# Optimization experiments

Measured on AMD Instinct MI355X. Metric: run time of the kernel, lower is better.

## Reference

```python
import jax, jax.numpy as jnp
import numpy as np


def gcn_conv(x, edge_index, W, b):
    # PyG GCNConv with normalize=True: add self-loops, symmetric D^-1/2 A D^-1/2,
    # transform then aggregate messages source->target, then add bias.
    N = x.shape[0]
    row, col = edge_index[0], edge_index[1]  # row: source, col: target
    loop = jnp.arange(N, dtype=edge_index.dtype)
    row = jnp.concatenate([row, loop])
    col = jnp.concatenate([col, loop])
    ones = jnp.ones(row.shape[0], dtype=x.dtype)
    deg = jax.ops.segment_sum(ones, col, num_segments=N)
    dinv = jnp.where(deg > 0, jax.lax.rsqrt(deg), 0.0)
    norm = dinv[row] * dinv[col]            # [E+N]
    h = x @ W                                # [N, d_out] transform first (cheaper aggregation)
    msgs = h[row] * norm[:, None]            # gather + scale
    out = jax.ops.segment_sum(msgs, col, num_segments=N)  # scatter-add to targets
    return out + b


def setup_inputs() -> dict:
    key = jax.random.key(0)
    k = jax.random.split(key, 6)
    N, D, H, C, E = 100000, 256, 32, 2, 3200000
    x = jax.random.normal(k[0], (N, D), dtype=jnp.float32)
    edge_index = jax.random.randint(k[1], (2, E), 0, N, dtype=jnp.int64)
    # glorot-style init for GCN weights
    W1 = jax.random.normal(k[2], (D, H), dtype=jnp.float32) * np.sqrt(2.0 / (D + H))
    b1 = jnp.zeros((H,), dtype=jnp.float32)
    W2 = jax.random.normal(k[3], (H, C), dtype=jnp.float32) * np.sqrt(2.0 / (H + C))
    b2 = jnp.zeros((C,), dtype=jnp.float32)
    return {"x": x, "edge_index": edge_index, "W1": W1, "b1": b1, "W2": W2, "b2": b2}


def reference(x, edge_index, W1, b1, W2, b2):
    # CRD: GCNConv -> relu -> dropout(p=0.5, eval mode -> identity)
    h = jax.nn.relu(gcn_conv(x, edge_index, W1, b1))
    # CLS: GCNConv -> log_softmax over classes
    logits = gcn_conv(h, edge_index, W2, b2)
    return jax.nn.log_softmax(logits, axis=1)
```

## Files before the change

kernel.cpp:

```cpp
#include <hip/hip_runtime.h>
#include <hip/hip_fp16.h>
#include <math.h>

#define DIV_UP(a,b) (((a)+(b)-1)/(b))

typedef _Float16 f16x8 __attribute__((ext_vector_type(8)));
typedef float    f32x4 __attribute__((ext_vector_type(4)));

#define SHIFT 9
#define TPB   (1 << SHIFT)
#define LMASK (TPB - 1)
#define CHUNK 4096

__global__ __launch_bounds__(256) void k_init(int* __restrict__ gcur, int cap,
                                              int* __restrict__ offsets, int N, int E) {
    const int t = threadIdx.x;
    gcur[t] = t * cap;
    if (t == 0) offsets[N] = E;
}

__global__ __launch_bounds__(256) void k_fat(const float* __restrict__ x,
                                             const float* __restrict__ W,
                                             __half* __restrict__ h1,
                                             const int* __restrict__ row,
                                             const int* __restrict__ col,
                                             int* __restrict__ gcur,
                                             unsigned* __restrict__ binned,
                                             int E, int N, int nchunk) {
    __shared__ __align__(16) char smem[24608];
    const int t = threadIdx.x;
    const int bid = blockIdx.x;
    const bool isBin = (bid < 2 * nchunk) && (bid & 1);

    if (!isBin) {
        const int gb = (bid < 2 * nchunk) ? (bid >> 1) : (bid - nchunk);
        _Float16* WlT = (_Float16*)smem;

#pragma unroll
        for (int i = 0; i < 8; ++i) {
            int idx = t + 256 * i;
            float4 v = ((const float4*)W)[idx];
            int k  = idx >> 3;
            int n4 = (idx & 7) * 4;
            int kc = k >> 5, q = (k >> 3) & 3, j = k & 7;
            int ct = n4 >> 4, m0 = n4 & 15;
            _Float16* dst = WlT + ((size_t)((kc * 2 + ct) * 64 + q * 16 + m0) * 8 + j);
            dst[0 * 8] = (_Float16)v.x;
            dst[1 * 8] = (_Float16)v.y;
            dst[2 * 8] = (_Float16)v.z;
            dst[3 * 8] = (_Float16)v.w;
        }
        __syncthreads();

        const int lane = t & 63;
        const int wv   = t >> 6;
        const int m    = lane & 15;
        const int q    = lane >> 4;

        const int rowA   = gb * 64 + wv * 16 + m;
        const int rclamp = min(rowA, N - 1);
        const float* xr  = x + (long long)rclamp * 256 + q * 8;

        f32x4 c0 = {0.f, 0.f, 0.f, 0.f}, c1 = {0.f, 0.f, 0.f, 0.f};
#pragma unroll
        for (int kc = 0; kc < 8; ++kc) {
            float4 v0 = *(const float4*)(xr + kc * 32);
            float4 v1 = *(const float4*)(xr + kc * 32 + 4);
            f16x8 b0 = *(const f16x8*)&WlT[(size_t)((kc * 2 + 0) * 64 + lane) * 8];
            f16x8 b1 = *(const f16x8*)&WlT[(size_t)((kc * 2 + 1) * 64 + lane) * 8];
            f16x8 a;
            a[0] = (_Float16)v0.x; a[1] = (_Float16)v0.y;
            a[2] = (_Float16)v0.z; a[3] = (_Float16)v0.w;
            a[4] = (_Float16)v1.x; a[5] = (_Float16)v1.y;
            a[6] = (_Float16)v1.z; a[7] = (_Float16)v1.w;
            c0 = __builtin_amdgcn_mfma_f32_16x16x32_f16(a, b0, c0, 0, 0, 0);
            c1 = __builtin_amdgcn_mfma_f32_16x16x32_f16(a, b1, c1, 0, 0, 0);
        }

        const int orow = gb * 64 + wv * 16 + q * 4;
#pragma unroll
        for (int r = 0; r < 4; ++r) {
            int gr = orow + r;
            if (gr < N) {
                h1[gr * 32 + m]      = __float2half(c0[r]);
                h1[gr * 32 + 16 + m] = __float2half(c1[r]);
            }
        }
    } else {
        int* hist  = (int*)smem;
        int* loff  = hist + 256;
        int* gbase = loff + 256;
        int* lcur  = gbase + 256;
        unsigned* staged     = (unsigned*)(smem + 4096);
        unsigned char* binOf = (unsigned char*)(smem + 4096 + 16384);
        int* wtot            = (int*)(smem + 4096 + 16384 + 4096);

        const int base = (bid >> 1) * CHUNK;
        const int n = min(CHUNK, E - base);

        hist[t] = 0;
        __syncthreads();

        unsigned pk[CHUNK / 256];
        int bn[CHUNK / 256];
#pragma unroll
        for (int k = 0; k < CHUNK / 256; ++k) {
            int i = base + t + k * 256;
            if (i < E) {
                int c = col[i], r = row[i];
                bn[k] = c >> SHIFT;
                pk[k] = ((unsigned)r << SHIFT) | (unsigned)(c & LMASK);
                atomicAdd(&hist[bn[k]], 1);
            } else bn[k] = -1;
        }
        __syncthreads();

        const int hv = hist[t];
        int sc = hv;
#pragma unroll
        for (int s = 1; s < 64; s <<= 1) {
            int y = __shfl_up(sc, s, 64);
            if ((t & 63) >= s) sc += y;
        }
        if ((t & 63) == 63) wtot[t >> 6] = sc;
        __syncthreads();
        int woff = 0;
#pragma unroll
        for (int j = 0; j < 3; ++j) if (j < (t >> 6)) woff += wtot[j];
        const int excl = sc + woff - hv;
        gbase[t] = hv ? atomicAdd(&gcur[t], hv) : 0;
        lcur[t] = excl;
        loff[t] = excl;
        __syncthreads();

#pragma unroll
        for (int k = 0; k < CHUNK / 256; ++k) {
            if (bn[k] >= 0) {
                int p = atomicAdd(&lcur[bn[k]], 1);
                staged[p] = pk[k];
                binOf[p] = (unsigned char)bn[k];
            }
        }
        __syncthreads();

        for (int i = t; i < n; i += 256) {
            int bb = binOf[i];
            binned[gbase[bb] + (i - loff[bb])] = staged[i];
        }
    }
}

__global__ __launch_bounds__(1024) void k_csr2(const unsigned* __restrict__ binned,
                                               const int* __restrict__ gcur, int cap,
                                               int* __restrict__ offsets,
                                               float* __restrict__ dinv,
                                               int* __restrict__ srcs,
                                               __half* __restrict__ h1, int N) {
    __shared__ int h[TPB];
    __shared__ int cur[TPB];
    __shared__ float sdi[TPB];
    __shared__ int wred[16];
    const int t = threadIdx.x, b = blockIdx.x;
    const int lane = t & 63, wv = t >> 6;
    const int beg = b * cap, end = gcur[b];

    int contrib = (t < 256 && t < b) ? (gcur[t] - t * cap) : 0;
#pragma unroll
    for (int s = 1; s < 64; s <<= 1) contrib += __shfl_xor(contrib, s, 64);
    if (t < TPB) h[t] = 0;
    if (lane == 0 && wv < 4) wred[wv] = contrib;
    __syncthreads();
    const int obase = wred[0] + wred[1] + wred[2] + wred[3];

    for (int i = beg + t; i < end; i += 1024)
        atomicAdd(&h[binned[i] & LMASK], 1);
    __syncthreads();

    const int cnt = (t < TPB) ? h[t] : 0;
    int sc = cnt;
#pragma unroll
    for (int s = 1; s < 64; s <<= 1) {
        int y = __shfl_up(sc, s, 64);
        if (lane >= s) sc += y;
    }
    if (t < TPB && lane == 63) wred[8 + wv] = sc;
    __syncthreads();
    if (t < TPB) {
        int woff = 0;
        for (int j = 0; j < wv; ++j) woff += wred[8 + j];
        const int excl = sc + woff - cnt;
        const int g = (b << SHIFT) + t;
        const int pos0 = obase + excl;
        float di = 0.f;
        if (g < N) {
            offsets[g] = pos0;
            di = rsqrtf((float)(1 + cnt));
            dinv[g] = di;
        }
        cur[t] = pos0;
        sdi[t] = di;
    }
    __syncthreads();

    for (int i = beg + t; i < end; i += 1024) {
        unsigned v = binned[i];
        int pos = atomicAdd(&cur[v & LMASK], 1);
        srcs[pos] = (int)(v >> SHIFT);
    }

    const int node = (b << SHIFT) + (t >> 1);
    if (node < N) {
        float di = sdi[t >> 1];
        uint4* hp4 = (uint4*)(h1 + (size_t)node * 32) + (t & 1) * 2;
#pragma unroll
        for (int k4 = 0; k4 < 2; ++k4) {
            uint4 v = hp4[k4];
            __half2* ph = (__half2*)&v;
#pragma unroll
            for (int k2 = 0; k2 < 4; ++k2) {
                float2 u = __half22float2(ph[k2]);
                ph[k2] = __floats2half2_rn(u.x * di, u.y * di);
            }
            hp4[k4] = v;
        }
    }
}

__global__ void k_agg1(const int* __restrict__ offsets, const int* __restrict__ srcs,
                       const float* __restrict__ dinv, const __half* __restrict__ h1w,
                       const float* __restrict__ b1, const float* __restrict__ W2,
                       __half2* __restrict__ tw, int N) {
    long long g = (long long)blockIdx.x * blockDim.x + threadIdx.x;
    int node = (int)(g >> 5), f = (int)(g & 31);
    if (node >= N) return;
    const int sub = f >> 2, q = f & 3;
    const int beg = offsets[node], end = offsets[node + 1];
    const uint4* h4 = (const uint4*)h1w;

    float a0 = 0.f, a1 = 0.f, a2 = 0.f, a3 = 0.f;
    float a4 = 0.f, a5 = 0.f, a6 = 0.f, a7 = 0.f;

    for (int j = beg; j < end; j += 16) {
        int e0 = j + sub, e1 = j + 8 + sub;
        int s0 = srcs[min(e0, end - 1)];
        int s1 = srcs[min(e1, end - 1)];
        float m0 = (e0 < end) ? 1.f : 0.f;
        float m1 = (e1 < end) ? 1.f : 0.f;
        uint4 rv0 = h4[s0 * 4 + q];
        uint4 rv1 = h4[s1 * 4 + q];
        __half2 p; float2 u;
        p = *(__half2*)&rv0.x; u = __half22float2(p); a0 = fmaf(u.x, m0, a0); a1 = fmaf(u.y, m0, a1);
        p = *(__half2*)&rv0.y; u = __half22float2(p); a2 = fmaf(u.x, m0, a2); a3 = fmaf(u.y, m0, a3);
        p = *(__half2*)&rv0.z; u = __half22float2(p); a4 = fmaf(u.x, m0, a4); a5 = fmaf(u.y, m0, a5);
        p = *(__half2*)&rv0.w; u = __half22float2(p); a6 = fmaf(u.x, m0, a6); a7 = fmaf(u.y, m0, a7);
        p = *(__half2*)&rv1.x; u = __half22float2(p); a0 = fmaf(u.x, m1, a0); a1 = fmaf(u.y, m1, a1);
        p = *(__half2*)&rv1.y; u = __half22float2(p); a2 = fmaf(u.x, m1, a2); a3 = fmaf(u.y, m1, a3);
        p = *(__half2*)&rv1.z; u = __half22float2(p); a4 = fmaf(u.x, m1, a4); a5 = fmaf(u.y, m1, a5);
        p = *(__half2*)&rv1.w; u = __half22float2(p); a6 = fmaf(u.x, m1, a6); a7 = fmaf(u.y, m1, a7);
    }
#pragma unroll
    for (int s = 4; s < 32; s <<= 1) {
        a0 += __shfl_xor(a0, s, 32); a1 += __shfl_xor(a1, s, 32);
        a2 += __shfl_xor(a2, s, 32); a3 += __shfl_xor(a3, s, 32);
        a4 += __shfl_xor(a4, s, 32); a5 += __shfl_xor(a5, s, 32);
        a6 += __shfl_xor(a6, s, 32); a7 += __shfl_xor(a7, s, 32);
    }
    if (sub == 0) {
        float di = dinv[node];
        uint4 rv = h4[node * 4 + q];
        float sf[8];
        {
            __half2 p; float2 u;
            p = *(__half2*)&rv.x; u = __half22float2(p); sf[0] = u.x; sf[1] = u.y;
            p = *(__half2*)&rv.y; u = __half22float2(p); sf[2] = u.x; sf[3] = u.y;
            p = *(__half2*)&rv.z; u = __half22float2(p); sf[4] = u.x; sf[5] = u.y;
            p = *(__half2*)&rv.w; u = __half22float2(p); sf[6] = u.x; sf[7] = u.y;
        }
        float av[8] = {a0, a1, a2, a3, a4, a5, a6, a7};
        float t0 = 0.f, t1 = 0.f;
#pragma unroll
        for (int k = 0; k < 8; ++k) {
            int feat = q * 8 + k;
            float hv = fmaf(di, av[k] + sf[k], b1[feat]);
            hv = fmaxf(hv, 0.f);
            t0 = fmaf(hv, W2[feat * 2 + 0], t0);
            t1 = fmaf(hv, W2[feat * 2 + 1], t1);
        }
        t0 += __shfl_xor(t0, 1, 32); t0 += __shfl_xor(t0, 2, 32);
        t1 += __shfl_xor(t1, 1, 32); t1 += __shfl_xor(t1, 2, 32);
        if (q == 0) tw[node] = __floats2half2_rn(di * t0, di * t1);
    }
}

__global__ __launch_bounds__(1024) void k_cls(const unsigned* __restrict__ binned,
                                              const int* __restrict__ gcur, int cap,
                                              const float* __restrict__ dinv,
                                              const __half2* __restrict__ tw,
                                              const float* __restrict__ b2,
                                              float* __restrict__ out, int N) {
    __shared__ float lacc[2 * TPB];
    const int t = threadIdx.x, b = blockIdx.x;
    lacc[t] = 0.f;
    __syncthreads();
    const int beg = b * cap, end = gcur[b];
    for (int i = beg + t; i < end; i += 1024) {
        unsigned v = binned[i];
        int loc = v & LMASK;
        float2 u = __half22float2(tw[v >> SHIFT]);
        atomicAdd(&lacc[2 * loc],     u.x);
        atomicAdd(&lacc[2 * loc + 1], u.y);
    }
    __syncthreads();
    if (t < TPB) {
        int g = (b << SHIFT) + t;
        if (g < N) {
            float di = dinv[g];
            float2 u = __half22float2(tw[g]);
            float z0 = di * (lacc[2 * t]     + u.x) + b2[0];
            float z1 = di * (lacc[2 * t + 1] + u.y) + b2[1];
            float m = fmaxf(z0, z1);
            float lse = m + logf(expf(z0 - m) + expf(z1 - m));
            ((float2*)out)[g] = float2{z0 - lse, z1 - lse};
        }
    }
}

extern "C" void kernel_launch(void* const* d_in, const int* in_sizes, int n_in,
                              void* d_out, int out_size, void* d_ws, size_t ws_size,
                              hipStream_t stream) {
    const float* x  = (const float*)d_in[0];
    const int*   ei = (const int*)d_in[1];
    const float* W1 = (const float*)d_in[2];
    const float* b1 = (const float*)d_in[3];
    const float* W2 = (const float*)d_in[4];
    const float* b2 = (const float*)d_in[5];

    const int H = in_sizes[3];
    const int D = in_sizes[2] / H;
    const int N = in_sizes[0] / D;
    const int E = in_sizes[1] / 2;
    (void)H; (void)n_in; (void)out_size; (void)ws_size;

    const int* row = ei;
    const int* col = ei + E;

    const int K_used = ((N - 1) >> SHIFT) + 1;
    const int cap    = (DIV_UP(E, K_used) * 5 / 4 + 255) & ~255;
    const int nchunk = DIV_UP(E, CHUNK);
    const int gemmB  = DIV_UP(N, 64);

    char* p = (char*)d_ws;
    auto alloc = [&](size_t bytes) { char* q = p; p += (bytes + 255) & ~(size_t)255; return q; };
    int*      offsets = (int*)     alloc((size_t)(N + 1) * 4);
    int*      gcur    = (int*)     alloc(256 * 4);
    float*    dinv    = (float*)   alloc((size_t)N * 4);
    unsigned* binned  = (unsigned*)alloc((size_t)K_used * cap * 4);
    __half*   h1      = (__half*)  alloc((size_t)N * 32 * 2);
    int*      srcs    = (int*)     alloc((size_t)E * 4);
    __half2*  tw      = (__half2*) alloc((size_t)N * 4);

    k_init <<<1, 256, 0, stream>>>(gcur, cap, offsets, N, E);
    k_fat  <<<gemmB + nchunk, 256, 0, stream>>>(x, W1, h1, row, col, gcur, binned, E, N, nchunk);
    k_csr2 <<<K_used, 1024, 0, stream>>>(binned, gcur, cap, offsets, dinv, srcs, h1, N);
    k_agg1 <<<(int)DIV_UP((long long)N * 32, 256), 256, 0, stream>>>(offsets, srcs, dinv, h1, b1, W2, tw, N);
    k_cls  <<<K_used, 1024, 0, stream>>>(binned, gcur, cap, dinv, tw, b2, (float*)d_out, N);
}
```

Baseline: 303.8 us.

## Split fused bin/GEMM kernel, compute degrees with global atomics, CSR-based layer-2 aggregation

Splits the combined binning and GEMM kernel into separate k_bin and k_gemm launches. Node degrees are now counted in k_bin with global atomics on a zeroed deg array, so the CSR kernel no longer builds a shared-memory histogram pass over binned edges. The GEMM preloads all x rows into registers before the MFMA loop, separated by a scheduling barrier. The second-layer aggregation now gathers over the CSR (offsets/srcs) with 16 threads per node instead of LDS float atomics over binned edges. In exchange, the bin and GEMM work no longer run concurrently, and 3.2M global atomics on deg are added.

```diff
diff --git a/kernel.cpp b/kernel.cpp
--- a/kernel.cpp
+++ b/kernel.cpp
@@ -13,150 +13,159 @@
 #define CHUNK 4096
 
 __global__ __launch_bounds__(256) void k_init(int* __restrict__ gcur, int cap,
-                                              int* __restrict__ offsets, int N, int E) {
-    const int t = threadIdx.x;
-    gcur[t] = t * cap;
-    if (t == 0) offsets[N] = E;
-}
-
-__global__ __launch_bounds__(256) void k_fat(const float* __restrict__ x,
-                                             const float* __restrict__ W,
-                                             __half* __restrict__ h1,
-                                             const int* __restrict__ row,
+                                              int* __restrict__ offsets,
+                                              int* __restrict__ deg, int N, int E) {
+    const int g = blockIdx.x * 256 + threadIdx.x;
+    if (g < N) deg[g] = 0;
+    if (blockIdx.x == 0) {
+        gcur[threadIdx.x] = threadIdx.x * cap;
+        if (threadIdx.x == 0) offsets[N] = E;
+    }
+}
+
+__global__ __launch_bounds__(256) void k_bin(const int* __restrict__ row,
                                              const int* __restrict__ col,
                                              int* __restrict__ gcur,
+                                             int* __restrict__ deg,
                                              unsigned* __restrict__ binned,
-                                             int E, int N, int nchunk) {
-    __shared__ __align__(16) char smem[24608];
+                                             int E) {
+    __shared__ int hist[256];
+    __shared__ int loff[256];
+    __shared__ int gbase[256];
+    __shared__ int lcur[256];
+    __shared__ unsigned staged[CHUNK];
+    __shared__ unsigned char binOf[CHUNK];
+    __shared__ int wtot[4];
+
     const int t = threadIdx.x;
-    const int bid = blockIdx.x;
-    const bool isBin = (bid < 2 * nchunk) && (bid & 1);
-
-    if (!isBin) {
-        const int gb = (bid < 2 * nchunk) ? (bid >> 1) : (bid - nchunk);
-        _Float16* WlT = (_Float16*)smem;
-
-#pragma unroll
-        for (int i = 0; i < 8; ++i) {
-            int idx = t + 256 * i;
-            float4 v = ((const float4*)W)[idx];
-            int k  = idx >> 3;
-            int n4 = (idx & 7) * 4;
-            int kc = k >> 5, q = (k >> 3) & 3, j = k & 7;
-            int ct = n4 >> 4, m0 = n4 & 15;
-            _Float16* dst = WlT + ((size_t)((kc * 2 + ct) * 64 + q * 16 + m0) * 8 + j);
-            dst[0 * 8] = (_Float16)v.x;
-            dst[1 * 8] = (_Float16)v.y;
-            dst[2 * 8] = (_Float16)v.z;
-            dst[3 * 8] = (_Float16)v.w;
-        }
-        __syncthreads();
-
-        const int lane = t & 63;
-        const int wv   = t >> 6;
-        const int m    = lane & 15;
-        const int q    = lane >> 4;
-
-        const int rowA   = gb * 64 + wv * 16 + m;
-        const int rclamp = min(rowA, N - 1);
-        const float* xr  = x + (long long)rclamp * 256 + q * 8;
-
-        f32x4 c0 = {0.f, 0.f, 0.f, 0.f}, c1 = {0.f, 0.f, 0.f, 0.f};
-#pragma unroll
-        for (int kc = 0; kc < 8; ++kc) {
-            float4 v0 = *(const float4*)(xr + kc * 32);
-            float4 v1 = *(const float4*)(xr + kc * 32 + 4);
-            f16x8 b0 = *(const f16x8*)&WlT[(size_t)((kc * 2 + 0) * 64 + lane) * 8];
-            f16x8 b1 = *(const f16x8*)&WlT[(size_t)((kc * 2 + 1) * 64 + lane) * 8];
-            f16x8 a;
-            a[0] = (_Float16)v0.x; a[1] = (_Float16)v0.y;
-            a[2] = (_Float16)v0.z; a[3] = (_Float16)v0.w;
-            a[4] = (_Float16)v1.x; a[5] = (_Float16)v1.y;
-            a[6] = (_Float16)v1.z; a[7] = (_Float16)v1.w;
-            c0 = __builtin_amdgcn_mfma_f32_16x16x32_f16(a, b0, c0, 0, 0, 0);
-            c1 = __builtin_amdgcn_mfma_f32_16x16x32_f16(a, b1, c1, 0, 0, 0);
-        }
-
-        const int orow = gb * 64 + wv * 16 + q * 4;
-#pragma unroll
-        for (int r = 0; r < 4; ++r) {
-            int gr = orow + r;
-            if (gr < N) {
-                h1[gr * 32 + m]      = __float2half(c0[r]);
-                h1[gr * 32 + 16 + m] = __float2half(c1[r]);
-            }
-        }
-    } else {
-        int* hist  = (int*)smem;
-        int* loff  = hist + 256;
-        int* gbase = loff + 256;
-        int* lcur  = gbase + 256;
-        unsigned* staged     = (unsigned*)(smem + 4096);
-        unsigned char* binOf = (unsigned char*)(smem + 4096 + 16384);
-        int* wtot            = (int*)(smem + 4096 + 16384 + 4096);
-
-        const int base = (bid >> 1) * CHUNK;
-        const int n = min(CHUNK, E - base);
-
-        hist[t] = 0;
-        __syncthreads();
-
-        unsigned pk[CHUNK / 256];
-        int bn[CHUNK / 256];
-#pragma unroll
-        for (int k = 0; k < CHUNK / 256; ++k) {
-            int i = base + t + k * 256;
-            if (i < E) {
-                int c = col[i], r = row[i];
-                bn[k] = c >> SHIFT;
-                pk[k] = ((unsigned)r << SHIFT) | (unsigned)(c & LMASK);
-                atomicAdd(&hist[bn[k]], 1);
-            } else bn[k] = -1;
-        }
-        __syncthreads();
-
-        const int hv = hist[t];
-        int sc = hv;
-#pragma unroll
-        for (int s = 1; s < 64; s <<= 1) {
-            int y = __shfl_up(sc, s, 64);
-            if ((t & 63) >= s) sc += y;
-        }
-        if ((t & 63) == 63) wtot[t >> 6] = sc;
-        __syncthreads();
-        int woff = 0;
-#pragma unroll
-        for (int j = 0; j < 3; ++j) if (j < (t >> 6)) woff += wtot[j];
-        const int excl = sc + woff - hv;
-        gbase[t] = hv ? atomicAdd(&gcur[t], hv) : 0;
-        lcur[t] = excl;
-        loff[t] = excl;
-        __syncthreads();
-
-#pragma unroll
-        for (int k = 0; k < CHUNK / 256; ++k) {
-            if (bn[k] >= 0) {
-                int p = atomicAdd(&lcur[bn[k]], 1);
-                staged[p] = pk[k];
-                binOf[p] = (unsigned char)bn[k];
-            }
-        }
-        __syncthreads();
-
-        for (int i = t; i < n; i += 256) {
-            int bb = binOf[i];
-            binned[gbase[bb] + (i - loff[bb])] = staged[i];
-        }
-    }
-}
-
-__global__ __launch_bounds__(1024) void k_csr2(const unsigned* __restrict__ binned,
-                                               const int* __restrict__ gcur, int cap,
-                                               int* __restrict__ offsets,
-                                               float* __restrict__ dinv,
-                                               int* __restrict__ srcs,
-                                               __half* __restrict__ h1, int N) {
-    __shared__ int h[TPB];
+    const int base = blockIdx.x * CHUNK;
+    const int n = min(CHUNK, E - base);
+
+    hist[t] = 0;
+    __syncthreads();
+
+    unsigned pk[CHUNK / 256];
+    int bn[CHUNK / 256];
+#pragma unroll
+    for (int k = 0; k < CHUNK / 256; ++k) {
+        int i = base + t + k * 256;
+        if (i < E) {
+            int c = col[i], r = row[i];
+            bn[k] = c >> SHIFT;
+            pk[k] = ((unsigned)r << SHIFT) | (unsigned)(c & LMASK);
+            atomicAdd(&hist[bn[k]], 1);
+            atomicAdd(&deg[c], 1);
+        } else bn[k] = -1;
+    }
+    __syncthreads();
+
+    const int hv = hist[t];
+    int sc = hv;
+#pragma unroll
+    for (int s = 1; s < 64; s <<= 1) {
+        int y = __shfl_up(sc, s, 64);
+        if ((t & 63) >= s) sc += y;
+    }
+    if ((t & 63) == 63) wtot[t >> 6] = sc;
+    __syncthreads();
+    int woff = 0;
+#pragma unroll
+    for (int j = 0; j < 3; ++j) if (j < (t >> 6)) woff += wtot[j];
+    const int excl = sc + woff - hv;
+    gbase[t] = hv ? atomicAdd(&gcur[t], hv) : 0;
+    lcur[t] = excl;
+    loff[t] = excl;
+    __syncthreads();
+
+#pragma unroll
+    for (int k = 0; k < CHUNK / 256; ++k) {
+        if (bn[k] >= 0) {
+            int p = atomicAdd(&lcur[bn[k]], 1);
+            staged[p] = pk[k];
+            binOf[p] = (unsigned char)bn[k];
+        }
+    }
+    __syncthreads();
+
+    for (int i = t; i < n; i += 256) {
+        int bb = binOf[i];
+        binned[gbase[bb] + (i - loff[bb])] = staged[i];
+    }
+}
+
+__global__ __launch_bounds__(256) void k_gemm(const float* __restrict__ x,
+                                              const float* __restrict__ W,
+                                              __half* __restrict__ h1, int N) {
+    __shared__ __align__(16) _Float16 WlT[8192];
+    const int t = threadIdx.x;
+    const int gb = blockIdx.x;
+
+#pragma unroll
+    for (int i = 0; i < 8; ++i) {
+        int idx = t + 256 * i;
+        float4 v = ((const float4*)W)[idx];
+        int k  = idx >> 3;
+        int n4 = (idx & 7) * 4;
+        int kc = k >> 5, q = (k >> 3) & 3, j = k & 7;
+        int ct = n4 >> 4, m0 = n4 & 15;
+        _Float16* dst = WlT + ((size_t)((kc * 2 + ct) * 64 + q * 16 + m0) * 8 + j);
+        dst[0 * 8] = (_Float16)v.x;
+        dst[1 * 8] = (_Float16)v.y;
+        dst[2 * 8] = (_Float16)v.z;
+        dst[3 * 8] = (_Float16)v.w;
+    }
+    __syncthreads();
+
+    const int lane = t & 63;
+    const int wv   = t >> 6;
+    const int m    = lane & 15;
+    const int q    = lane >> 4;
+
+    const int rowA   = gb * 64 + wv * 16 + m;
+    const int rclamp = min(rowA, N - 1);
+    const float* xr  = x + (long long)rclamp * 256 + q * 8;
+
+    float4 va[16];
+#pragma unroll
+    for (int kc = 0; kc < 8; ++kc) {
+        va[2 * kc]     = *(const float4*)(xr + kc * 32);
+        va[2 * kc + 1] = *(const float4*)(xr + kc * 32 + 4);
+    }
+    __builtin_amdgcn_sched_barrier(0);
+
+    f32x4 c0 = {0.f, 0.f, 0.f, 0.f}, c1 = {0.f, 0.f, 0.f, 0.f};
+#pragma unroll
+    for (int kc = 0; kc < 8; ++kc) {
+        f16x8 b0 = *(const f16x8*)&WlT[(size_t)((kc * 2 + 0) * 64 + lane) * 8];
+        f16x8 b1 = *(const f16x8*)&WlT[(size_t)((kc * 2 + 1) * 64 + lane) * 8];
+        float4 v0 = va[2 * kc], v1 = va[2 * kc + 1];
+        f16x8 a;
+        a[0] = (_Float16)v0.x; a[1] = (_Float16)v0.y;
+        a[2] = (_Float16)v0.z; a[3] = (_Float16)v0.w;
+        a[4] = (_Float16)v1.x; a[5] = (_Float16)v1.y;
+        a[6] = (_Float16)v1.z; a[7] = (_Float16)v1.w;
+        c0 = __builtin_amdgcn_mfma_f32_16x16x32_f16(a, b0, c0, 0, 0, 0);
+        c1 = __builtin_amdgcn_mfma_f32_16x16x32_f16(a, b1, c1, 0, 0, 0);
+    }
+
+    const int orow = gb * 64 + wv * 16 + q * 4;
+#pragma unroll
+    for (int r = 0; r < 4; ++r) {
+        int gr = orow + r;
+        if (gr < N) {
+            h1[gr * 32 + m]      = __float2half(c0[r]);
+            h1[gr * 32 + 16 + m] = __float2half(c1[r]);
+        }
+    }
+}
+
+__global__ __launch_bounds__(1024) void k_csr(const unsigned* __restrict__ binned,
+                                              const int* __restrict__ gcur, int cap,
+                                              const int* __restrict__ deg,
+                                              int* __restrict__ offsets,
+                                              float* __restrict__ dinv,
+                                              int* __restrict__ srcs,
+                                              __half* __restrict__ h1, int N) {
     __shared__ int cur[TPB];
     __shared__ float sdi[TPB];
     __shared__ int wred[16];
@@ -167,16 +176,13 @@
     int contrib = (t < 256 && t < b) ? (gcur[t] - t * cap) : 0;
 #pragma unroll
     for (int s = 1; s < 64; s <<= 1) contrib += __shfl_xor(contrib, s, 64);
-    if (t < TPB) h[t] = 0;
     if (lane == 0 && wv < 4) wred[wv] = contrib;
     __syncthreads();
     const int obase = wred[0] + wred[1] + wred[2] + wred[3];
 
-    for (int i = beg + t; i < end; i += 1024)
-        atomicAdd(&h[binned[i] & LMASK], 1);
-    __syncthreads();
-
-    const int cnt = (t < TPB) ? h[t] : 0;
+    const int g = (b << SHIFT) + t;
+    const int cnt = (t < TPB && g < N) ? deg[g] : 0;
+
     int sc = cnt;
 #pragma unroll
     for (int s = 1; s < 64; s <<= 1) {
@@ -189,7 +195,6 @@
         int woff = 0;
         for (int j = 0; j < wv; ++j) woff += wred[8 + j];
         const int excl = sc + woff - cnt;
-        const int g = (b << SHIFT) + t;
         const int pos0 = obase + excl;
         float di = 0.f;
         if (g < N) {
@@ -292,36 +297,33 @@
     }
 }
 
-__global__ __launch_bounds__(1024) void k_cls(const unsigned* __restrict__ binned,
-                                              const int* __restrict__ gcur, int cap,
-                                              const float* __restrict__ dinv,
-                                              const __half2* __restrict__ tw,
-                                              const float* __restrict__ b2,
-                                              float* __restrict__ out, int N) {
-    __shared__ float lacc[2 * TPB];
-    const int t = threadIdx.x, b = blockIdx.x;
-    lacc[t] = 0.f;
-    __syncthreads();
-    const int beg = b * cap, end = gcur[b];
-    for (int i = beg + t; i < end; i += 1024) {
-        unsigned v = binned[i];
-        int loc = v & LMASK;
-        float2 u = __half22float2(tw[v >> SHIFT]);
-        atomicAdd(&lacc[2 * loc],     u.x);
-        atomicAdd(&lacc[2 * loc + 1], u.y);
-    }
-    __syncthreads();
-    if (t < TPB) {
-        int g = (b << SHIFT) + t;
-        if (g < N) {
-            float di = dinv[g];
-            float2 u = __half22float2(tw[g]);
-            float z0 = di * (lacc[2 * t]     + u.x) + b2[0];
-            float z1 = di * (lacc[2 * t + 1] + u.y) + b2[1];
-            float m = fmaxf(z0, z1);
-            float lse = m + logf(expf(z0 - m) + expf(z1 - m));
-            ((float2*)out)[g] = float2{z0 - lse, z1 - lse};
-        }
+__global__ void k_agg2(const int* __restrict__ offsets, const int* __restrict__ srcs,
+                       const float* __restrict__ dinv, const __half2* __restrict__ tw,
+                       const float* __restrict__ b2, float* __restrict__ out, int N) {
+    long long g = (long long)blockIdx.x * blockDim.x + threadIdx.x;
+    int node = (int)(g >> 4), f = (int)(g & 15);
+    if (node >= N) return;
+    int beg = offsets[node], end = offsets[node + 1];
+    float a0 = 0.f, a1 = 0.f;
+    for (int j = beg + f; j < end; j += 16) {
+        int s = srcs[j];
+        float2 u = __half22float2(tw[s]);
+        a0 += u.x;
+        a1 += u.y;
+    }
+#pragma unroll
+    for (int s = 8; s; s >>= 1) {
+        a0 += __shfl_xor(a0, s, 64);
+        a1 += __shfl_xor(a1, s, 64);
+    }
+    if (f == 0) {
+        float di = dinv[node];
+        float2 u = __half22float2(tw[node]);
+        float z0 = di * (a0 + u.x) + b2[0];
+        float z1 = di * (a1 + u.y) + b2[1];
+        float m = fmaxf(z0, z1);
+        float lse = m + logf(expf(z0 - m) + expf(z1 - m));
+        ((float2*)out)[node] = float2{z0 - lse, z1 - lse};
     }
 }
 
@@ -353,15 +355,17 @@
     auto alloc = [&](size_t bytes) { char* q = p; p += (bytes + 255) & ~(size_t)255; return q; };
     int*      offsets = (int*)     alloc((size_t)(N + 1) * 4);
     int*      gcur    = (int*)     alloc(256 * 4);
+    int*      deg     = (int*)     alloc((size_t)N * 4);
     float*    dinv    = (float*)   alloc((size_t)N * 4);
     unsigned* binned  = (unsigned*)alloc((size_t)K_used * cap * 4);
     __half*   h1      = (__half*)  alloc((size_t)N * 32 * 2);
     int*      srcs    = (int*)     alloc((size_t)E * 4);
     __half2*  tw      = (__half2*) alloc((size_t)N * 4);
 
-    k_init <<<1, 256, 0, stream>>>(gcur, cap, offsets, N, E);
-    k_fat  <<<gemmB + nchunk, 256, 0, stream>>>(x, W1, h1, row, col, gcur, binned, E, N, nchunk);
-    k_csr2 <<<K_used, 1024, 0, stream>>>(binned, gcur, cap, offsets, dinv, srcs, h1, N);
+    k_init <<<DIV_UP(N, 256), 256, 0, stream>>>(gcur, cap, offsets, deg, N, E);
+    k_bin  <<<nchunk, 256, 0, stream>>>(row, col, gcur, deg, binned, E);
+    k_gemm <<<gemmB, 256, 0, stream>>>(x, W1, h1, N);
+    k_csr  <<<K_used, 1024, 0, stream>>>(binned, gcur, cap, deg, offsets, dinv, srcs, h1, N);
     k_agg1 <<<(int)DIV_UP((long long)N * 32, 256), 256, 0, stream>>>(offsets, srcs, dinv, h1, b1, W2, tw, N);
-    k_cls  <<<K_used, 1024, 0, stream>>>(binned, gcur, cap, dinv, tw, b2, (float*)d_out, N);
-}
+    k_agg2 <<<(int)DIV_UP((long long)N * 16, 256), 256, 0, stream>>>(offsets, srcs, dinv, tw, b2, (float*)d_out, N);
+}
```

Measured after the change: 405.4 us. 1.33x slower.
